# Performance work log

Measured on AMD Instinct MI355X. Metric: run time of the kernel, lower is better.

The kernel has to match this reference:

```python
import jax, jax.numpy as jnp
import numpy as np

B, N, E, V, L, H, FF = 8, 256, 512, 512, 4, 8, 2048
PAD = 0

def _layernorm(x, g, b):
    m = x.mean(-1, keepdims=True)
    v = ((x - m) ** 2).mean(-1, keepdims=True)
    return (x - m) / jnp.sqrt(v + 1e-5) * g + b


def setup_inputs() -> dict:
    key = jax.random.key(0)
    ks = jax.random.split(key, 20)
    s = 0.02
    inp = {
        'src_tokens': jax.random.randint(ks[0], (B, N), 1, V),  # avoid pad id 0
        'padded_coordinates': jax.random.normal(ks[1], (B, N, 3), jnp.float32),
        'src_distance': jax.random.uniform(ks[2], (B, N, N), jnp.float32) * 10.0,
        'src_edge_type': jax.random.randint(ks[3], (B, N, N), 0, 32),
        'embed': (jax.random.normal(ks[4], (V, E), jnp.float32) * s).at[PAD].set(0.0),
        'dp_w1': jax.random.normal(ks[5], (E, 1), jnp.float32) * s,
        'dp_b1': jnp.zeros((E,), jnp.float32),
        'dp_w2': jax.random.normal(ks[6], (1, E), jnp.float32) * s,
        'dp_b2': jnp.zeros((1,), jnp.float32),
        'Wqkv': jax.random.normal(ks[7], (L, 3 * E, E), jnp.float32) * s,
        'bqkv': jnp.zeros((L, 3 * E), jnp.float32),
        'Wo': jax.random.normal(ks[8], (L, E, E), jnp.float32) * s,
        'bo': jnp.zeros((L, E), jnp.float32),
        'ln1_g': jnp.ones((L, E), jnp.float32),
        'ln1_b': jnp.zeros((L, E), jnp.float32),
        'W1': jax.random.normal(ks[9], (L, FF, E), jnp.float32) * s,
        'b1': jnp.zeros((L, FF), jnp.float32),
        'W2': jax.random.normal(ks[10], (L, E, FF), jnp.float32) * s,
        'b2': jnp.zeros((L, E), jnp.float32),
        'ln2_g': jnp.ones((L, E), jnp.float32),
        'ln2_b': jnp.zeros((L, E), jnp.float32),
    }
    return inp


def reference(src_tokens, padded_coordinates, src_distance, src_edge_type,
              embed, dp_w1, dp_b1, dp_w2, dp_b2,
              Wqkv, bqkv, Wo, bo, ln1_g, ln1_b, W1, b1, W2, b2, ln2_g, ln2_b):
    pad_mask = src_tokens == PAD  # [B,N] bool
    x = embed[src_tokens]  # [B,N,E]

    # dist_proj: Linear(1,E) -> tanh -> Linear(E,1) on [B,N,N,1]
    h = jnp.tanh(src_distance[..., None] * dp_w1[:, 0] + dp_b1)  # [B,N,N,E]
    bias = jnp.einsum('bqke,e->bqk', h, dp_w2[0]) + dp_b2[0]      # [B,N,N]
    bias = jnp.where(pad_mask[:, None, :], -jnp.inf, bias)
    bias = jnp.where(pad_mask[:, :, None], -jnp.inf, bias)

    dh = E // H
    scale = 1.0 / jnp.sqrt(jnp.float32(dh))
    nl = Wqkv.shape[0]
    for l in range(nl):
        qkv = x @ Wqkv[l].T + bqkv[l]
        q, k, v = jnp.split(qkv, 3, axis=-1)
        q = q.reshape(B, N, H, dh).transpose(0, 2, 1, 3)
        k = k.reshape(B, N, H, dh).transpose(0, 2, 1, 3)
        v = v.reshape(B, N, H, dh).transpose(0, 2, 1, 3)
        scores = jnp.einsum('bhqd,bhkd->bhqk', q, k) * scale + bias[:, None]
        a = jax.nn.softmax(scores, axis=-1)
        o = jnp.einsum('bhqk,bhkd->bhqd', a, v).transpose(0, 2, 1, 3).reshape(B, N, E)
        x = _layernorm(x + o @ Wo[l].T + bo[l], ln1_g[l], ln1_b[l])
        ff = jax.nn.gelu(x @ W1[l].T + b1[l], approximate=False) @ W2[l].T + b2[l]
        x = _layernorm(x + ff, ln2_g[l], ln2_b[l])
    return x, pad_mask
```

## Files before the change

### kernel.cpp

```cpp
#include <hip/hip_runtime.h>
#include <hip/hip_bf16.h>


namespace {
constexpr int Bn  = 8;
constexpr int Nn  = 256;
constexpr int En  = 512;
constexpr int Ln  = 4;
constexpr int Hn  = 8;
constexpr int FFn = 2048;
constexpr int DHn = 64;
constexpr int Mn  = Bn * Nn;
constexpr int QKV_LD = 3 * En;
constexpr int LUT_N = 4096;
}

typedef float f32x4 __attribute__((ext_vector_type(4)));
typedef short bf16x8 __attribute__((ext_vector_type(8)));

__device__ __forceinline__ unsigned short f2bs(float f) {
    union { float f; unsigned u; } v; v.f = f;
    unsigned r = v.u + 0x7FFFu + ((v.u >> 16) & 1u);
    return (unsigned short)(r >> 16);
}
__device__ __forceinline__ float bf2f(short s) {
    union { unsigned u; float f; } v;
    v.u = ((unsigned)(unsigned short)s) << 16;
    return v.f;
}

__device__ __forceinline__ int swz(int row, int byte_in_row, int stride_b) {
    return row * stride_b + (byte_in_row ^ ((row & 7) << 4));
}

struct CvtArgs {
    const float* src[4];
    unsigned short* dst[4];
    int n4[4];
    int blkoff[5];
};
__global__ __launch_bounds__(256) void k_cvt(CvtArgs a) {
    int bid = blockIdx.x;
    int r = 0;
    if (bid >= a.blkoff[1]) r = 1;
    if (bid >= a.blkoff[2]) r = 2;
    if (bid >= a.blkoff[3]) r = 3;
    int i = (bid - a.blkoff[r]) * 256 + threadIdx.x;
    if (i >= a.n4[r]) return;
    f32x4 v = *(const f32x4*)(a.src[r] + (size_t)i * 4);
    unsigned short o[4] = {f2bs(v[0]), f2bs(v[1]), f2bs(v[2]), f2bs(v[3])};
    *(unsigned long long*)(a.dst[r] + (size_t)i * 4) = *(unsigned long long*)o;
}

__global__ __launch_bounds__(256) void k_embed_lut(const int* __restrict__ tok,
                                                   const float* __restrict__ emb,
                                                   float* __restrict__ x,
                                                   unsigned short* __restrict__ xb,
                                                   const float* __restrict__ w1,
                                                   const float* __restrict__ b1,
                                                   const float* __restrict__ w2,
                                                   float* __restrict__ lut) {
    constexpr int EMB_BLOCKS = Mn * En / 256;
    if (blockIdx.x < EMB_BLOCKS) {
        int i = blockIdx.x * 256 + threadIdx.x;
        int m = i >> 9;
        int e = i & 511;
        float v = emb[tok[m] * En + e];
        x[i] = v;
        xb[i] = f2bs(v);
        return;
    }
    __shared__ float sw1[En], sb1[En], sw2[En];
    for (int e = threadIdx.x; e < En; e += 256) {
        sw1[e] = w1[e]; sb1[e] = b1[e]; sw2[e] = w2[e];
    }
    __syncthreads();
    int i = (blockIdx.x - EMB_BLOCKS) * 256 + threadIdx.x;
    if (i > LUT_N) return;
    float d = (float)i * (10.0f / (float)LUT_N);
    float acc = 0.f;
#pragma unroll 4
    for (int e = 0; e < En; ++e) {
        float s = fmaf(d, sw1[e], sb1[e]);
        float t = 1.f - 2.f / (__expf(2.f * s) + 1.f);
        acc = fmaf(t, sw2[e], acc);
    }
    lut[i] = acc;
}

__global__ __launch_bounds__(256) void k_distbias_lut(const float* __restrict__ dist,
                                                      const int* __restrict__ tok,
                                                      const float* __restrict__ lut,
                                                      const float* __restrict__ b2,
                                                      float* __restrict__ biasmat) {
    int i = blockIdx.x * 256 + threadIdx.x;
    float d = dist[i];
    float idx = d * ((float)LUT_N / 10.0f);
    int ii = (int)idx;
    ii = ii < 0 ? 0 : (ii > LUT_N - 1 ? LUT_N - 1 : ii);
    float frac = idx - (float)ii;
    float v0 = lut[ii], v1 = lut[ii + 1];
    float acc = fmaf(v1 - v0, frac, v0) + b2[0];
    int k = i & (Nn - 1);
    int q = (i >> 8) & (Nn - 1);
    int b = i >> 16;
    bool pad = (tok[b * Nn + k] == 0) || (tok[b * Nn + q] == 0);
    biasmat[i] = pad ? -1e30f : acc;
}

__global__ __launch_bounds__(256, 1) void k_attn(
        const unsigned short* __restrict__ qkvb,
        const float* __restrict__ biasmat,
        unsigned short* __restrict__ attnb) {
    __shared__ short Qs[64 * 64];
    __shared__ short Ks[256 * 64];
    __shared__ short Vs[64 * 256];
    __shared__ short Ps[64 * 256];

    const int tid = threadIdx.x;
    const int lane = tid & 63;
    const int wv = tid >> 6;
    const int q0 = blockIdx.x * 64;
    const int bh = blockIdx.y;
    const int b = bh >> 3, h = bh & 7;

    const unsigned short* Qg = qkvb + ((size_t)(b * Nn + q0)) * QKV_LD + h * DHn;
    const unsigned short* Kg = qkvb + ((size_t)(b * Nn)) * QKV_LD + En + h * DHn;
    const unsigned short* VgR = qkvb + ((size_t)(b * Nn)) * QKV_LD + 2 * En + h * DHn;

    {
        const char* src = (const char*)(Kg + (size_t)tid * QKV_LD);
#pragma unroll
        for (int c = 0; c < 8; ++c)
            *(bf16x8*)((char*)Ks + swz(tid, c * 16, 128)) =
                *(const bf16x8*)(src + c * 16);
    }
    {
        const char* src = (const char*)(VgR + (size_t)tid * QKV_LD);
#pragma unroll
        for (int c = 0; c < 8; ++c) {
            bf16x8 v = *(const bf16x8*)(src + c * 16);
#pragma unroll
            for (int j = 0; j < 8; ++j) {
                int d = c * 8 + j;
                *(short*)((char*)Vs + (d * 512 + ((tid * 2) ^ ((d & 7) << 4)))) = v[j];
            }
        }
    }
    {
        int r = tid & 63;
        const char* src = (const char*)(Qg + (size_t)r * QKV_LD);
#pragma unroll
        for (int i = 0; i < 2; ++i) {
            int cb = ((tid >> 6) * 2 + i) * 16;
            bf16x8 v = *(const bf16x8*)(src + cb);
            bf16x8 o;
#pragma unroll
            for (int j = 0; j < 8; ++j) o[j] = (short)f2bs(bf2f(v[j]) * 0.125f);
            *(bf16x8*)((char*)Qs + swz(r, cb, 128)) = o;
        }
    }

    const int qw = wv * 16;
    const int g  = lane >> 4;
    const int c  = lane & 15;
    f32x4 acc[16];
    {
        const float* bb = biasmat + ((size_t)b * Nn + (q0 + qw + g * 4)) * Nn;
#pragma unroll
        for (int f = 0; f < 16; ++f)
#pragma unroll
            for (int r = 0; r < 4; ++r)
                acc[f][r] = bb[(size_t)r * Nn + f * 16 + c];
    }

    __syncthreads();

    bf16x8 qa[2];
#pragma unroll
    for (int ks = 0; ks < 2; ++ks)
        qa[ks] = *(const bf16x8*)((const char*)Qs + swz(qw + c, ks * 64 + g * 16, 128));
#pragma unroll
    for (int f = 0; f < 16; ++f) {
#pragma unroll
        for (int ks = 0; ks < 2; ++ks) {
            bf16x8 kb = *(const bf16x8*)((const char*)Ks +
                         swz(f * 16 + c, ks * 64 + g * 16, 128));
            acc[f] = __builtin_amdgcn_mfma_f32_16x16x32_bf16(qa[ks], kb, acc[f], 0, 0, 0);
        }
    }

    float rcp[4];
#pragma unroll
    for (int r = 0; r < 4; ++r) {
        float m = acc[0][r];
#pragma unroll
        for (int f = 1; f < 16; ++f) m = fmaxf(m, acc[f][r]);
#pragma unroll
        for (int o = 1; o < 16; o <<= 1) m = fmaxf(m, __shfl_xor(m, o));
        float s = 0.f;
#pragma unroll
        for (int f = 0; f < 16; ++f) {
            float e = __expf(acc[f][r] - m);
            acc[f][r] = e;
            s += e;
        }
#pragma unroll
        for (int o = 1; o < 16; o <<= 1) s += __shfl_xor(s, o);
        rcp[r] = 1.f / s;
    }

#pragma unroll
    for (int f = 0; f < 16; ++f)
#pragma unroll
        for (int r = 0; r < 4; ++r) {
            int q = qw + g * 4 + r;
            int kx = f * 16 + c;
            *(unsigned short*)((char*)Ps + (q * 512 + ((kx * 2) ^ ((q & 7) << 4)))) =
                f2bs(acc[f][r] * rcp[r]);
        }

    f32x4 acc2[4];
#pragma unroll
    for (int fd = 0; fd < 4; ++fd) acc2[fd] = {0.f, 0.f, 0.f, 0.f};
#pragma unroll
    for (int ks2 = 0; ks2 < 8; ++ks2) {
        bf16x8 pa = *(const bf16x8*)((const char*)Ps +
                      swz(qw + c, ks2 * 64 + g * 16, 512));
#pragma unroll
        for (int fd = 0; fd < 4; ++fd) {
            bf16x8 vb = *(const bf16x8*)((const char*)Vs +
                          swz(fd * 16 + c, ks2 * 64 + g * 16, 512));
            acc2[fd] = __builtin_amdgcn_mfma_f32_16x16x32_bf16(pa, vb, acc2[fd], 0, 0, 0);
        }
    }

    unsigned short* Cg = attnb + ((size_t)(b * Nn + q0 + qw)) * En + h * DHn;
#pragma unroll
    for (int fd = 0; fd < 4; ++fd)
#pragma unroll
        for (int r = 0; r < 4; ++r)
            Cg[(size_t)(g * 4 + r) * En + fd * 16 + c] = f2bs(acc2[fd][r]);
}

template <int BM, int BN, int BK, int MODE, int CBF>
__global__ __launch_bounds__(256) void k_gemm(
        const unsigned short* __restrict__ A, int lda,
        const unsigned short* __restrict__ Bw, int ldb,
        const float* __restrict__ bias,
        void* __restrict__ Cp, int ldc, long long sCz,
        int K) {
    static_assert(BM == BN, "square tiles only");
    constexpr int LDS_S = BK + 8;
    constexpr int WM = BM / 2, WN = BN / 2;
    constexpr int FM = WM / 16, FN = WN / 16;
    constexpr int GR = 256 / BM;
    constexpr int TC = BK / GR;
    constexpr int NR = TC / 8;

    __shared__ short As[BM * LDS_S];
    __shared__ short Bs[BM * LDS_S];

    const int tid  = threadIdx.x;
    const int lane = tid & 63;
    const int wv   = tid >> 6;
    const int wr   = wv >> 1, wc = wv & 1;
    const int m0 = blockIdx.x * BM, n0 = blockIdx.y * BN;
    const int z  = blockIdx.z;

    const int arow = tid / GR;
    const int acol = (tid % GR) * TC;

    const unsigned short* Abase = A  + (size_t)(m0 + arow) * lda + (size_t)z * K + acol;
    const unsigned short* Bbase = Bw + (size_t)(n0 + arow) * ldb + (size_t)z * K + acol;

    bf16x8 pa[NR], pb[NR];
#pragma unroll
    for (int i = 0; i < NR; ++i) pa[i] = *(const bf16x8*)(Abase + 8 * i);
#pragma unroll
    for (int i = 0; i < NR; ++i) pb[i] = *(const bf16x8*)(Bbase + 8 * i);

    f32x4 acc[FM][FN];
#pragma unroll
    for (int i = 0; i < FM; ++i)
#pragma unroll
        for (int j = 0; j < FN; ++j) acc[i][j] = {0.f, 0.f, 0.f, 0.f};

    const int fk   = (lane >> 4) * 8;
    const int frow = lane & 15;
    short* awp = &As[arow * LDS_S + acol];
    short* bwp = &Bs[arow * LDS_S + acol];

    const int nt = K / BK;
    for (int t = 0; t < nt; ++t) {
#pragma unroll
        for (int i = 0; i < NR; ++i) *(bf16x8*)(awp + i * 8) = pa[i];
#pragma unroll
        for (int i = 0; i < NR; ++i) *(bf16x8*)(bwp + i * 8) = pb[i];
        __syncthreads();

        if (t + 1 < nt) {
            const unsigned short* An = Abase + (size_t)(t + 1) * BK;
            const unsigned short* Bn = Bbase + (size_t)(t + 1) * BK;
#pragma unroll
            for (int i = 0; i < NR; ++i) pa[i] = *(const bf16x8*)(An + 8 * i);
#pragma unroll
            for (int i = 0; i < NR; ++i) pb[i] = *(const bf16x8*)(Bn + 8 * i);
        }

#pragma unroll
        for (int ks = 0; ks < BK / 32; ++ks) {
            bf16x8 af[FM], bfr[FN];
#pragma unroll
            for (int i = 0; i < FM; ++i)
                af[i] = *(const bf16x8*)&As[(wr * WM + i * 16 + frow) * LDS_S + ks * 32 + fk];
#pragma unroll
            for (int j = 0; j < FN; ++j)
                bfr[j] = *(const bf16x8*)&Bs[(wc * WN + j * 16 + frow) * LDS_S + ks * 32 + fk];
#pragma unroll
            for (int i = 0; i < FM; ++i)
#pragma unroll
                for (int j = 0; j < FN; ++j)
                    acc[i][j] = __builtin_amdgcn_mfma_f32_16x16x32_bf16(
                        af[i], bfr[j], acc[i][j], 0, 0, 0);
        }
        __syncthreads();
    }

#pragma unroll
    for (int i = 0; i < FM; ++i) {
#pragma unroll
        for (int j = 0; j < FN; ++j) {
            const int n = n0 + wc * WN + j * 16 + (lane & 15);
            float bv = 0.f;
            if constexpr (MODE == 0 || MODE == 1) bv = bias[n];
#pragma unroll
            for (int r = 0; r < 4; ++r) {
                const int m = m0 + wr * WM + i * 16 + (lane >> 4) * 4 + r;
                float v = acc[i][j][r] + bv;
                if constexpr (MODE == 1)
                    v = 0.5f * v * (1.f + erff(v * 0.70710678118654752f));
                if constexpr (CBF)
                    ((unsigned short*)Cp)[(size_t)m * ldc + n] = f2bs(v);
                else
                    ((float*)Cp)[(size_t)z * sCz + (size_t)m * ldc + n] = v;
            }
        }
    }
}

template <int FINAL>
__global__ __launch_bounds__(256) void k_addln(
        const float* __restrict__ xin,
        const float* __restrict__ yp, long long ystride, int nsplit,
        const float* __restrict__ biasv,
        const float* __restrict__ g, const float* __restrict__ bb,
        float* __restrict__ xout, unsigned short* __restrict__ xbf,
        const int* __restrict__ tok) {
    const int row = blockIdx.x;
    const int tid = threadIdx.x;
    const size_t base = (size_t)row * En;
    float v0 = xin[base + tid] + biasv[tid];
    float v1 = xin[base + tid + 256] + biasv[tid + 256];
    for (int s = 0; s < nsplit; ++s) {
        v0 += yp[(size_t)s * ystride + base + tid];
        v1 += yp[(size_t)s * ystride + base + tid + 256];
    }
    float s1 = v0 + v1;
    float s2 = v0 * v0 + v1 * v1;
#pragma unroll
    for (int o = 32; o; o >>= 1) {
        s1 += __shfl_xor(s1, o);
        s2 += __shfl_xor(s2, o);
    }
    __shared__ float ws1[4], ws2[4];
    int w = tid >> 6;
    if ((tid & 63) == 0) { ws1[w] = s1; ws2[w] = s2; }
    __syncthreads();
    s1 = (ws1[0] + ws1[1]) + (ws1[2] + ws1[3]);
    s2 = (ws2[0] + ws2[1]) + (ws2[2] + ws2[3]);
    const float rE = 1.f / (float)En;
    float mean = s1 * rE;
    float var = s2 * rE - mean * mean;
    float inv = rsqrtf(var + 1e-5f);
    float o0 = (v0 - mean) * inv * g[tid] + bb[tid];
    float o1 = (v1 - mean) * inv * g[tid + 256] + bb[tid + 256];
    xout[base + tid]       = o0;
    xout[base + tid + 256] = o1;
    if constexpr (FINAL) {
        if (tid == 0)
            xout[(size_t)Mn * En + row] = (tok[row] == 0) ? 1.f : 0.f;
    } else {
        xbf[base + tid]       = f2bs(o0);
        xbf[base + tid + 256] = f2bs(o1);
    }
}

extern "C" void kernel_launch(void* const* d_in, const int* in_sizes, int n_in,
                              void* d_out, int out_size, void* d_ws, size_t ws_size,
                              hipStream_t stream) {
    const int*   tok   = (const int*)  d_in[0];
    const float* dist  = (const float*)d_in[2];
    const float* emb   = (const float*)d_in[4];
    const float* dp_w1 = (const float*)d_in[5];
    const float* dp_b1 = (const float*)d_in[6];
    const float* dp_w2 = (const float*)d_in[7];
    const float* dp_b2 = (const float*)d_in[8];
    const float* Wqkv  = (const float*)d_in[9];
    const float* bqkv  = (const float*)d_in[10];
    const float* Wo    = (const float*)d_in[11];
    const float* bo    = (const float*)d_in[12];
    const float* ln1g  = (const float*)d_in[13];
    const float* ln1b  = (const float*)d_in[14];
    const float* W1    = (const float*)d_in[15];
    const float* b1    = (const float*)d_in[16];
    const float* W2    = (const float*)d_in[17];
    const float* b2    = (const float*)d_in[18];
    const float* ln2g  = (const float*)d_in[19];
    const float* ln2b  = (const float*)d_in[20];

    char* p = (char*)d_ws;
    float*          biasmat = (float*)p;          p += (size_t)Bn*Nn*Nn*4;
    float*          x       = (float*)p;          p += (size_t)Mn*En*4;
    unsigned short* xb      = (unsigned short*)p; p += (size_t)Mn*En*2;
    unsigned short* qkvb    = (unsigned short*)p; p += (size_t)Mn*QKV_LD*2;
    unsigned short* Sffb    = (unsigned short*)p; p += (size_t)Mn*FFn*2;
    unsigned short* attnb   = (unsigned short*)p; p += (size_t)Mn*En*2;
    float*          yp      = (float*)p;          p += (size_t)4*Mn*En*4;
    float*          lut     = (float*)p;          p += (size_t)(LUT_N+8)*4;
    unsigned short* wqkvb   = (unsigned short*)p; p += (size_t)Ln*QKV_LD*En*2;
    unsigned short* wob     = (unsigned short*)p; p += (size_t)Ln*En*En*2;
    unsigned short* w1b     = (unsigned short*)p; p += (size_t)Ln*FFn*En*2;
    unsigned short* w2b     = (unsigned short*)p; p += (size_t)Ln*En*FFn*2;

    {
        CvtArgs a;
        a.src[0] = Wqkv; a.dst[0] = wqkvb; a.n4[0] = Ln * QKV_LD * En / 4;
        a.src[1] = Wo;   a.dst[1] = wob;   a.n4[1] = Ln * En * En / 4;
        a.src[2] = W1;   a.dst[2] = w1b;   a.n4[2] = Ln * FFn * En / 4;
        a.src[3] = W2;   a.dst[3] = w2b;   a.n4[3] = Ln * En * FFn / 4;
        a.blkoff[0] = 0;
        for (int i = 0; i < 4; ++i)
            a.blkoff[i + 1] = a.blkoff[i] + (a.n4[i] + 255) / 256;
        k_cvt<<<a.blkoff[4], 256, 0, stream>>>(a);
    }

    k_embed_lut<<<Mn * En / 256 + (LUT_N + 256) / 256, 256, 0, stream>>>(
        tok, emb, x, xb, dp_w1, dp_b1, dp_w2, lut);
    k_distbias_lut<<<Bn * Nn * Nn / 256, 256, 0, stream>>>(dist, tok, lut, dp_b2,
                                                           biasmat);

    const long long yps = (long long)Mn * En;
    for (int l = 0; l < Ln; ++l) {
        const unsigned short* Wqkv_l = wqkvb + (size_t)l * QKV_LD * En;
        const float*          bqkv_l = bqkv  + (size_t)l * QKV_LD;
        const unsigned short* Wo_l   = wob   + (size_t)l * En * En;
        const unsigned short* W1_l   = w1b   + (size_t)l * FFn * En;
        const float*          b1_l   = b1    + (size_t)l * FFn;
        const unsigned short* W2_l   = w2b   + (size_t)l * En * FFn;

        k_gemm<64, 64, 128, 0, 1>
            <<<dim3(Mn / 64, QKV_LD / 64), 256, 0, stream>>>(
            xb, En, Wqkv_l, En, bqkv_l, qkvb, QKV_LD, 0, En);

        k_attn<<<dim3(Nn / 64, Bn * Hn), 256, 0, stream>>>(qkvb, biasmat, attnb);

        k_gemm<64, 64, 128, 3, 0>
            <<<dim3(Mn / 64, En / 64, 2), 256, 0, stream>>>(
            attnb, En, Wo_l, En, nullptr, yp, En, yps, En / 2);
        k_addln<0><<<Mn, 256, 0, stream>>>(x, yp, yps, 2,
                                           bo + (size_t)l * En,
                                           ln1g + (size_t)l * En, ln1b + (size_t)l * En,
                                           x, xb, tok);

        k_gemm<64, 64, 128, 1, 1>
            <<<dim3(Mn / 64, FFn / 64), 256, 0, stream>>>(
            xb, En, W1_l, En, b1_l, Sffb, FFn, 0, En);

        k_gemm<64, 64, 128, 3, 0>
            <<<dim3(Mn / 64, En / 64, 4), 256, 0, stream>>>(
            Sffb, FFn, W2_l, FFn, nullptr, yp, En, yps, FFn / 4);

        if (l < Ln - 1) {
            k_addln<0><<<Mn, 256, 0, stream>>>(x, yp, yps, 4,
                                               b2 + (size_t)l * En,
                                               ln2g + (size_t)l * En, ln2b + (size_t)l * En,
                                               x, xb, tok);
        } else {
            k_addln<1><<<Mn, 256, 0, stream>>>(x, yp, yps, 4,
                                               b2 + (size_t)l * En,
                                               ln2g + (size_t)l * En, ln2b + (size_t)l * En,
                                               (float*)d_out, nullptr, tok);
        }
    }
}
```

Baseline: 316.0 us.

## Load GEMM tiles directly into LDS with swizzled layout via global_load_lds

Replaces the register-staged global-to-LDS copy in the GEMM kernel with direct global_load_lds 16-byte transfers. The tile is stored in an XOR-swizzled layout instead of a padded one, to avoid bank conflicts on fragment reads. The goal is to cut VGPR pressure and the extra LDS store instructions. The register prefetch of the next K tile is dropped, so global load latency is no longer overlapped with MFMA work, and the kernel is now fixed to 64x64x128 tiles.

After: 295.6 us. -6.5%, faster.

```diff
diff --git a/kernel.cpp b/kernel.cpp
--- a/kernel.cpp
+++ b/kernel.cpp
@@ -31,6 +31,13 @@
 
 __device__ __forceinline__ int swz(int row, int byte_in_row, int stride_b) {
     return row * stride_b + (byte_in_row ^ ((row & 7) << 4));
+}
+
+__device__ __forceinline__ void gload_lds16(const void* g, void* l) {
+    __builtin_amdgcn_global_load_lds(
+        (const __attribute__((address_space(1))) unsigned int*)g,
+        (__attribute__((address_space(3))) unsigned int*)l,
+        16, 0, 0);
 }
 
 struct CvtArgs {
@@ -250,16 +257,9 @@
         const float* __restrict__ bias,
         void* __restrict__ Cp, int ldc, long long sCz,
         int K) {
-    static_assert(BM == BN, "square tiles only");
-    constexpr int LDS_S = BK + 8;
-    constexpr int WM = BM / 2, WN = BN / 2;
-    constexpr int FM = WM / 16, FN = WN / 16;
-    constexpr int GR = 256 / BM;
-    constexpr int TC = BK / GR;
-    constexpr int NR = TC / 8;
-
-    __shared__ short As[BM * LDS_S];
-    __shared__ short Bs[BM * LDS_S];
+    static_assert(BM == 64 && BN == 64 && BK == 128, "fixed geometry");
+    __shared__ short As[64 * 128];
+    __shared__ short Bs[64 * 128];
 
     const int tid  = threadIdx.x;
     const int lane = tid & 63;
@@ -268,59 +268,53 @@
     const int m0 = blockIdx.x * BM, n0 = blockIdx.y * BN;
     const int z  = blockIdx.z;
 
-    const int arow = tid / GR;
-    const int acol = (tid % GR) * TC;
-
-    const unsigned short* Abase = A  + (size_t)(m0 + arow) * lda + (size_t)z * K + acol;
-    const unsigned short* Bbase = Bw + (size_t)(n0 + arow) * ldb + (size_t)z * K + acol;
-
-    bf16x8 pa[NR], pb[NR];
-#pragma unroll
-    for (int i = 0; i < NR; ++i) pa[i] = *(const bf16x8*)(Abase + 8 * i);
-#pragma unroll
-    for (int i = 0; i < NR; ++i) pb[i] = *(const bf16x8*)(Bbase + 8 * i);
-
-    f32x4 acc[FM][FN];
-#pragma unroll
-    for (int i = 0; i < FM; ++i)
-#pragma unroll
-        for (int j = 0; j < FN; ++j) acc[i][j] = {0.f, 0.f, 0.f, 0.f};
-
-    const int fk   = (lane >> 4) * 8;
+    const int r_in = lane >> 4;
+    const int ch   = lane & 15;
+
+    f32x4 acc[2][2];
+#pragma unroll
+    for (int i = 0; i < 2; ++i)
+#pragma unroll
+        for (int j = 0; j < 2; ++j) acc[i][j] = {0.f, 0.f, 0.f, 0.f};
+
+    const int fkb  = (lane >> 4) * 16;
     const int frow = lane & 15;
-    short* awp = &As[arow * LDS_S + acol];
-    short* bwp = &Bs[arow * LDS_S + acol];
-
+
+    const size_t koff = (size_t)z * K;
     const int nt = K / BK;
     for (int t = 0; t < nt; ++t) {
-#pragma unroll
-        for (int i = 0; i < NR; ++i) *(bf16x8*)(awp + i * 8) = pa[i];
-#pragma unroll
-        for (int i = 0; i < NR; ++i) *(bf16x8*)(bwp + i * 8) = pb[i];
+        const size_t cb = (koff + (size_t)t * BK) * 2;
+#pragma unroll
+        for (int i = 0; i < 4; ++i) {
+            const int tr = wv * 16 + i * 4 + r_in;
+            const char* ga = (const char*)A +
+                (size_t)(m0 + tr) * lda * 2 + cb + ((ch ^ (tr & 7)) << 4);
+            gload_lds16(ga, &As[(wv * 16 + i * 4) * 128]);
+        }
+#pragma unroll
+        for (int i = 0; i < 4; ++i) {
+            const int tr = wv * 16 + i * 4 + r_in;
+            const char* gb = (const char*)Bw +
+                (size_t)(n0 + tr) * ldb * 2 + cb + ((ch ^ (tr & 7)) << 4);
+            gload_lds16(gb, &Bs[(wv * 16 + i * 4) * 128]);
+        }
         __syncthreads();
 
-        if (t + 1 < nt) {
-            const unsigned short* An = Abase + (size_t)(t + 1) * BK;
-            const unsigned short* Bn = Bbase + (size_t)(t + 1) * BK;
-#pragma unroll
-            for (int i = 0; i < NR; ++i) pa[i] = *(const bf16x8*)(An + 8 * i);
-#pragma unroll
-            for (int i = 0; i < NR; ++i) pb[i] = *(const bf16x8*)(Bn + 8 * i);
-        }
-
-#pragma unroll
-        for (int ks = 0; ks < BK / 32; ++ks) {
-            bf16x8 af[FM], bfr[FN];
-#pragma unroll
-            for (int i = 0; i < FM; ++i)
-                af[i] = *(const bf16x8*)&As[(wr * WM + i * 16 + frow) * LDS_S + ks * 32 + fk];
-#pragma unroll
-            for (int j = 0; j < FN; ++j)
-                bfr[j] = *(const bf16x8*)&Bs[(wc * WN + j * 16 + frow) * LDS_S + ks * 32 + fk];
-#pragma unroll
-            for (int i = 0; i < FM; ++i)
-#pragma unroll
-                for (int j = 0; j < FN; ++j)
+#pragma unroll
+        for (int ks = 0; ks < 4; ++ks) {
+            bf16x8 af[2], bfr[2];
+#pragma unroll
+            for (int i = 0; i < 2; ++i)
+                af[i] = *(const bf16x8*)((const char*)As +
+                         swz(wr * 32 + i * 16 + frow, ks * 64 + fkb, 256));
+#pragma unroll
+            for (int j = 0; j < 2; ++j)
+                bfr[j] = *(const bf16x8*)((const char*)Bs +
+                          swz(wc * 32 + j * 16 + frow, ks * 64 + fkb, 256));
+#pragma unroll
+            for (int i = 0; i < 2; ++i)
+#pragma unroll
+                for (int j = 0; j < 2; ++j)
                     acc[i][j] = __builtin_amdgcn_mfma_f32_16x16x32_bf16(
                         af[i], bfr[j], acc[i][j], 0, 0, 0);
         }
@@ -328,15 +322,15 @@
     }
 
 #pragma unroll
-    for (int i = 0; i < FM; ++i) {
-#pragma unroll
-        for (int j = 0; j < FN; ++j) {
-            const int n = n0 + wc * WN + j * 16 + (lane & 15);
+    for (int i = 0; i < 2; ++i) {
+#pragma unroll
+        for (int j = 0; j < 2; ++j) {
+            const int n = n0 + wc * 32 + j * 16 + (lane & 15);
             float bv = 0.f;
             if constexpr (MODE == 0 || MODE == 1) bv = bias[n];
 #pragma unroll
             for (int r = 0; r < 4; ++r) {
-                const int m = m0 + wr * WM + i * 16 + (lane >> 4) * 4 + r;
+                const int m = m0 + wr * 32 + i * 16 + (lane >> 4) * 4 + r;
                 float v = acc[i][j][r] + bv;
                 if constexpr (MODE == 1)
                     v = 0.5f * v * (1.f + erff(v * 0.70710678118654752f));
```
